# Optimization experiments

Hardware: AMD Instinct MI355X
Metric: run time of the kernel (lower is better)

Reference implementation:

```python
import jax, jax.numpy as jnp
import numpy as np

H, DM, N, K, R = 768, 1536, 16, 4, 48  # hidden, intermediate, state, conv kernel, dt rank
B, L = 2, 1024


def _silu(x):
    return x * jax.nn.sigmoid(x)


def _causal_conv(x, w, b):
    # x: [B, D, L]; w: [D, K] depthwise; causal left-pad K-1 (matches causal_conv1d_fn)
    out = jax.lax.conv_general_dilated(
        x, w[:, None, :], window_strides=(1,), padding=[(K - 1, 0)],
        feature_group_count=w.shape[0], dimension_numbers=('NCH', 'OIH', 'NCH'))
    return out + b[None, :, None]


def _selective_scan(u, delta, A, Bm, Cm, Dp, gate):
    # u/delta/gate: [B, D, L]; A: [D, N]; Bm/Cm: [B, L, N]; Dp: [D]
    dA = jnp.exp(delta[:, :, :, None] * A[None, :, None, :])              # [B,D,L,N]
    dBu = delta[:, :, :, None] * Bm[:, None, :, :] * u[:, :, :, None]      # [B,D,L,N]
    dA_t = jnp.moveaxis(dA, 2, 0)    # [L,B,D,N]
    dBu_t = jnp.moveaxis(dBu, 2, 0)  # [L,B,D,N]
    C_t = jnp.moveaxis(Cm, 1, 0)     # [L,B,N]

    def step(x, inp):
        a, bu, c = inp
        x = a * x + bu                               # [B,D,N]
        y = jnp.einsum('bdn,bn->bd', x, c)
        return x, y

    x0 = jnp.zeros(dA_t.shape[1:], dA_t.dtype)
    _, ys = jax.lax.scan(step, x0, (dA_t, dBu_t, C_t))
    y = jnp.moveaxis(ys, 0, 2) + u * Dp[None, :, None]   # [B,D,L]
    return y * _silu(gate)


def _branch(conv_out, gate, xw, dtw, dtb, Alog, Dp):
    # conv_out/gate: [B, D, L]
    ssm = jnp.einsum('bdl,pd->blp', conv_out, xw)        # [B,L,R+2N]
    ts, Bm, Cm = ssm[..., :R], ssm[..., R:R + N], ssm[..., R + N:]
    delta = jax.nn.softplus(jnp.einsum('dr,blr->bdl', dtw, ts) + dtb[None, :, None])
    A = -jnp.exp(Alog)
    return _selective_scan(conv_out, delta, A, Bm, Cm, Dp, gate)


def setup_inputs() -> dict:
    key = jax.random.key(0)
    ks = jax.random.split(key, 12)
    s = 0.02
    hidden_states = jax.random.normal(ks[0], (B, L, H), jnp.float32)
    in_proj_w = jax.random.normal(ks[1], (2 * DM, H), jnp.float32) * s
    conv_w = jax.random.normal(ks[2], (DM, K), jnp.float32) * 0.3
    conv_b = jax.random.normal(ks[3], (DM,), jnp.float32) * s
    x_proj_w = jax.random.normal(ks[4], (R + 2 * N, DM), jnp.float32) * s
    dt_proj_w = jax.random.normal(ks[5], (DM, R), jnp.float32) * s
    dt_proj_b = -4.0 + 0.1 * jax.random.normal(ks[6], (DM,), jnp.float32)
    x_proj_back_w = jax.random.normal(ks[7], (R + 2 * N, DM), jnp.float32) * s
    dt_proj_back_w = jax.random.normal(ks[8], (DM, R), jnp.float32) * s
    dt_proj_back_b = -4.0 + 0.1 * jax.random.normal(ks[9], (DM,), jnp.float32)
    A_log = jnp.log(jnp.broadcast_to(jnp.arange(1, N + 1, dtype=jnp.float32)[None, :], (DM, N)))
    A_log_back = A_log
    D = jnp.ones((DM,), jnp.float32)
    D_back = jnp.ones((DM,), jnp.float32)
    out_proj_w = jax.random.normal(ks[10], (H, DM), jnp.float32) * s
    return {
        'hidden_states': hidden_states, 'in_proj_w': in_proj_w,
        'conv_w': conv_w, 'conv_b': conv_b,
        'x_proj_w': x_proj_w, 'dt_proj_w': dt_proj_w, 'dt_proj_b': dt_proj_b,
        'x_proj_back_w': x_proj_back_w, 'dt_proj_back_w': dt_proj_back_w,
        'dt_proj_back_b': dt_proj_back_b, 'A_log': A_log, 'A_log_back': A_log_back,
        'D': D, 'D_back': D_back, 'out_proj_w': out_proj_w,
    }


def reference(hidden_states, in_proj_w, conv_w, conv_b, x_proj_w, dt_proj_w,
              dt_proj_b, x_proj_back_w, dt_proj_back_w, dt_proj_back_b,
              A_log, A_log_back, D, D_back, out_proj_w):
    proj = jnp.einsum('blh,ph->bpl', hidden_states, in_proj_w)  # [B,2D,L]
    x, gate = proj[:, :DM], proj[:, DM:]
    conv_out = _silu(_causal_conv(x, conv_w, conv_b))           # [B,D,L]
    # forward-direction scan
    y_f = _branch(conv_out, gate, x_proj_w, dt_proj_w, dt_proj_b, A_log, D)
    # backward-direction scan on time-flipped conv output and gate
    y_b = _branch(conv_out[:, :, ::-1], gate[:, :, ::-1], x_proj_back_w,
                  dt_proj_back_w, dt_proj_back_b, A_log_back, D_back)
    y = y_f + y_b[:, :, ::-1]
    return jnp.einsum('bdl,hd->blh', y, out_proj_w)
```

## Files before the change

### kernel.cpp

```cpp
#include <hip/hip_runtime.h>
#include <math.h>

constexpr int cH  = 768;
constexpr int cDM = 1536;
constexpr int cN  = 16;
constexpr int cR  = 48;
constexpr int cB  = 2;
constexpr int cL  = 1024;
constexpr int cPS = 160;
constexpr int cCK = 32;

typedef unsigned short u16;
typedef __attribute__((ext_vector_type(8))) short bf16x8;
typedef __attribute__((ext_vector_type(4))) float f32x4;

__device__ __forceinline__ u16 f2bf(float f) {
    unsigned u = __float_as_uint(f);
    u += 0x7FFF + ((u >> 16) & 1);
    return (u16)(u >> 16);
}
__device__ __forceinline__ float bf2f(u16 h) {
    return __uint_as_float((unsigned)h << 16);
}
__device__ __forceinline__ float fexp2(float x) {
    float r; asm("v_exp_f32 %0, %1" : "=v"(r) : "v"(x)); return r;
}
constexpr float cLOG2E = 1.44269504f;

__global__ __launch_bounds__(256)
void prep_kernel(const float* __restrict__ hid, const float* __restrict__ inw,
                 const float* __restrict__ xpw, const float* __restrict__ xpbw,
                 const float* __restrict__ outw, const float* __restrict__ dtw,
                 const float* __restrict__ dtbw,
                 u16* __restrict__ hid_b, u16* __restrict__ inw_b,
                 u16* __restrict__ xpw2_b, u16* __restrict__ outw_b,
                 u16* __restrict__ dtw2_b)
{
    const long i8 = ((long)blockIdx.x * 256 + threadIdx.x) * 8;
    const long e0 = 1572864;
    const long e1 = e0 + 2359296;
    const long e2 = e1 + 122880;
    const long e3 = e2 + 122880;
    const long e4 = e3 + 1179648;
    const long e5 = e4 + 98304;
    const long e6 = e5 + 98304;
    const float* in; u16* out; long off; int pad = 0;
    if      (i8 < e0) { in = hid;  out = hid_b;           off = i8; }
    else if (i8 < e1) { in = inw;  out = inw_b;           off = i8 - e0; }
    else if (i8 < e2) { in = xpw;  out = xpw2_b;          off = i8 - e1; }
    else if (i8 < e3) { in = xpbw; out = xpw2_b + 122880; off = i8 - e2; }
    else if (i8 < e4) { in = outw; out = outw_b;          off = i8 - e3; }
    else if (i8 < e5) { in = dtw;  out = dtw2_b;          off = i8 - e4; pad = 1; }
    else if (i8 < e6) { in = dtbw; out = dtw2_b + 98304;  off = i8 - e5; pad = 1; }
    else return;
    u16 o[8];
    if (!pad) {
        const float4 a = *(const float4*)&in[off];
        const float4 b = *(const float4*)&in[off + 4];
        o[0]=f2bf(a.x); o[1]=f2bf(a.y); o[2]=f2bf(a.z); o[3]=f2bf(a.w);
        o[4]=f2bf(b.x); o[5]=f2bf(b.y); o[6]=f2bf(b.z); o[7]=f2bf(b.w);
    } else {
        const long r = off >> 6; const int k0 = (int)(off & 63);
        #pragma unroll
        for (int k = 0; k < 8; ++k)
            o[k] = (k0 + k < cR) ? f2bf(in[r * cR + k0 + k]) : (u16)0;
    }
    *(uint4*)&out[off] = *(uint4*)o;
}

__global__ __launch_bounds__(256)
void tspad_kernel(const float* __restrict__ ssms, u16* __restrict__ out) {
    int i = blockIdx.x * 256 + threadIdx.x;
    int dirsel = i >> 17;
    int rem = i & 131071;
    int bl = rem >> 6, k = rem & 63;
    out[i] = (k < cR) ? f2bf(ssms[(long)bl * cPS + dirsel * 80 + k]) : (u16)0;
}

__global__ __launch_bounds__(256)
void comb_kernel(u16* __restrict__ yf, const u16* __restrict__ yb, long n8) {
    long i = (long)blockIdx.x * 256 + threadIdx.x;
    if (i >= n8) return;
    uint4 av = ((uint4*)yf)[i];
    uint4 bv = ((const uint4*)yb)[i];
    unsigned* ap = (unsigned*)&av;
    unsigned* bp = (unsigned*)&bv;
    #pragma unroll
    for (int j = 0; j < 4; ++j) {
        const float lo = bf2f((u16)(ap[j] & 0xffff)) + bf2f((u16)(bp[j] & 0xffff));
        const float hi = bf2f((u16)(ap[j] >> 16))    + bf2f((u16)(bp[j] >> 16));
        ap[j] = (unsigned)f2bf(lo) | ((unsigned)f2bf(hi) << 16);
    }
    ((uint4*)yf)[i] = av;
}

__device__ __forceinline__ void gld_lds16(const u16* g, u16* l) {
    __builtin_amdgcn_global_load_lds(
        (const __attribute__((address_space(1))) unsigned int*)g,
        (__attribute__((address_space(3))) unsigned int*)l, 16, 0, 0);
}

#define GST(SA, SB, k0) do {                                                   \
    _Pragma("unroll")                                                          \
    for (int h = 0; h < 3; ++h) {                                              \
        const int q  = wid * 3 + h;                                            \
        const int rw = lane >> 2;                                              \
        if (q < 4) {                                                           \
            const int r  = q * 16 + rw;                                        \
            const int sw = (r & 3) ^ ((r >> 2) & 3);                           \
            const int kg = (k0) + (((lane & 3) ^ sw) << 3);                    \
            gld_lds16(Ab + (long)(m0 + r) * lda + kg, &SA[q * 512]);           \
        } else {                                                               \
            const int r  = (q - 4) * 16 + rw;                                  \
            const int sw = (r & 3) ^ ((r >> 2) & 3);                           \
            const int kg = (k0) + (((lane & 3) ^ sw) << 3);                    \
            int nr = n0 + r; if (nr > N2 - 1) nr = N2 - 1;                     \
            gld_lds16(Bb + (long)nr * ldb + kg, &SB[(q - 4) * 512]);           \
        }                                                                      \
    }                                                                          \
} while (0)

#define CMP(SA, SB) do {                                                       \
    bf16x8 af[4], bfr[2];                                                      \
    _Pragma("unroll")                                                          \
    for (int i = 0; i < 4; ++i) {                                              \
        const int ra  = i * 16 + lr;                                           \
        const int swa = (ra & 3) ^ ((ra >> 2) & 3);                            \
        af[i] = *(const bf16x8*)&SA[ra * 32 + ((lc ^ swa) << 3)];              \
    }                                                                          \
    _Pragma("unroll")                                                          \
    for (int j = 0; j < 2; ++j) {                                              \
        const int rb  = wn + j * 16 + lr;                                      \
        const int swb = (rb & 3) ^ ((rb >> 2) & 3);                            \
        bfr[j] = *(const bf16x8*)&SB[rb * 32 + ((lc ^ swb) << 3)];             \
    }                                                                          \
    _Pragma("unroll")                                                          \
    for (int i = 0; i < 4; ++i)                                                \
        _Pragma("unroll")                                                      \
        for (int j = 0; j < 2; ++j)                                            \
            acc[i][j] = __builtin_amdgcn_mfma_f32_16x16x32_bf16(af[i], bfr[j], acc[i][j], 0, 0, 0); \
} while (0)

template<int EPI>
__global__ __launch_bounds__(256, 4)
void gemm_mfma(const u16* __restrict__ A, const u16* __restrict__ B,
               float* __restrict__ C0, float* __restrict__ C1,
               const float* __restrict__ bias,
               int N2, int Kd, int lda, int ldb, int ldc,
               long sA, long sC, int splitCol, int kspl)
{
    __shared__ __align__(16) u16 shA0[2048];
    __shared__ __align__(16) u16 shA1[2048];
    __shared__ __align__(16) u16 shB0[4096];
    __shared__ __align__(16) u16 shB1[4096];
    const int tid  = threadIdx.x;
    const int wid  = tid >> 6, lane = tid & 63;
    const int lr   = lane & 15, lc = lane >> 4;
    const int z    = blockIdx.z;
    const int bz   = z / kspl, ks = z % kspl;
    const int kpc  = Kd / kspl;
    const int kbeg = ks * kpc;
    const int nt   = kpc / 32;
    const int n0 = blockIdx.x * 128, m0 = blockIdx.y * 64;
    const int wn = wid * 32;

    const u16* Ab = A + (long)bz * sA;
    const u16* Bb = B;

    f32x4 acc[4][2] = {};

    GST(shA0, shB0, kbeg);
    __syncthreads();
    int t = 0;
    for (;;) {
        if (t + 1 < nt) GST(shA1, shB1, kbeg + (t + 1) * 32);
        CMP(shA0, shB0);
        __syncthreads();
        if (++t >= nt) break;
        if (t + 1 < nt) GST(shA0, shB0, kbeg + (t + 1) * 32);
        CMP(shA1, shB1);
        __syncthreads();
        if (++t >= nt) break;
    }

    #pragma unroll
    for (int i = 0; i < 4; ++i) {
        #pragma unroll
        for (int e = 0; e < 4; ++e) {
            const int m = m0 + i * 16 + lc * 4 + e;
            float* base0 = C0 + (long)bz * sC + (long)m * ldc;
            float* base1 = (C1 != nullptr) ? C1 + (long)bz * sC + (long)m * ldc : nullptr;
            #pragma unroll
            for (int j = 0; j < 2; ++j) {
                const int n = n0 + wn + j * 16 + lr;
                if (n < N2) {
                    float v = acc[i][j][e];
                    if (EPI == 1) {
                        const float t2 = v + bias[n];
                        v = fmaxf(t2, 0.f) + __logf(1.f + __expf(-fabsf(t2)));
                    }
                    float* cp = (base1 && n >= splitCol) ? base1 + (n - splitCol)
                                                         : base0 + n;
                    if (EPI == 2) atomicAdd(cp, v);
                    else          *cp = v;
                }
            }
        }
    }
}

__global__ __launch_bounds__(256)
void conv_silu2(const float* __restrict__ x, const float* __restrict__ cw,
                const float* __restrict__ cb,
                float* __restrict__ convTf, u16* __restrict__ convT_b)
{
    __shared__ float xt[35][64];
    const int l0 = blockIdx.x * 32, d0 = blockIdx.y * 64, b = blockIdx.z;
    const int tid = threadIdx.x;
    for (int i = tid; i < 35 * 64; i += 256) {
        const int r = i >> 6, c = i & 63;
        const int l = l0 - 3 + r;
        xt[r][c] = (l >= 0) ? x[((long)b * cL + l) * cDM + d0 + c] : 0.f;
    }
    __syncthreads();
    const int dc = tid & 63, lsub = tid >> 6;
    const int d = d0 + dc;
    const float w0 = cw[d*4], w1 = cw[d*4+1], w2 = cw[d*4+2], w3 = cw[d*4+3];
    const float bi = cb[d];
    #pragma unroll
    for (int k = 0; k < 8; ++k) {
        const int row = lsub * 8 + k;
        float v = bi;
        v = fmaf(w0, xt[row][dc],     v);
        v = fmaf(w1, xt[row + 1][dc], v);
        v = fmaf(w2, xt[row + 2][dc], v);
        v = fmaf(w3, xt[row + 3][dc], v);
        const float s = v / (1.f + __expf(-v));
        const long o = ((long)b * cL + l0 + row) * cDM + d;
        convTf[o] = s;
        convT_b[o] = f2bf(s);
    }
}

#define SA_LOAD(g, DU, UU) _Pragma("unroll")                                   \
    for (int k = 0; k < 4; ++k) {                                              \
        const int t_ = (g) * 4 + k;                                            \
        const int l_ = dir ? (base - t_) : (base + t_);                        \
        DU[k] = dT[(long)l_ * cDM + d]; UU[k] = uT[(long)l_ * cDM + d];        \
    }

#define SA_COMP(g, DU, UU) _Pragma("unroll")                                   \
    for (int k = 0; k < 4; ++k) {                                              \
        const int t_ = (g) * 4 + k;                                            \
        const float du_ = DU[k]; const float duu_ = du_ * UU[k];               \
        sdu += du_;                                                            \
        const float4 b0_ = *(const float4*)&bcA[t_][half * 8];                 \
        const float4 b1_ = *(const float4*)&bcA[t_][half * 8 + 4];             \
        const float bb_[8] = {b0_.x,b0_.y,b0_.z,b0_.w,b1_.x,b1_.y,b1_.z,b1_.w};\
        _Pragma("unroll")                                                      \
        for (int n = 0; n < 8; ++n)                                            \
            xs[n] = fmaf(fexp2(du_ * a2[n]), xs[n], duu_ * bb_[n]);            \
    }

__global__ __launch_bounds__(64, 4)
void scanA_kernel(const float* __restrict__ dT0, const float* __restrict__ dT1,
                  const float* __restrict__ uF, const float* __restrict__ ssms,
                  const float* __restrict__ AlogF, const float* __restrict__ AlogB,
                  float* __restrict__ Ap_out, float* __restrict__ Xf_out)
{
    __shared__ float bcA[32][16];
    const int lane = threadIdx.x;
    const int dd = lane & 31, half = lane >> 5;
    const int d = blockIdx.x * 32 + dd;
    const int b = blockIdx.y;
    const int z = blockIdx.z;
    const int dir = z >> 5, ck = z & 31;
    const float* Alog = dir ? AlogB : AlogF;
    const float* dT = (dir ? dT1 : dT0) + (long)b * cL * cDM;
    const float* uT = uF + (long)b * cL * cDM;
    const float* sp = ssms + (long)b * cL * cPS;
    const int sofs = dir ? 128 : 48;
    const int base = dir ? (cL - 1 - ck * 32) : (ck * 32);

    #pragma unroll
    for (int h = 0; h < 2; ++h) {
        const int idx = h * 64 + lane;
        const int r = idx >> 2, q = idx & 3;
        const int lr_ = dir ? (base - r) : (base + r);
        *(float4*)&bcA[r][q * 4] = *(const float4*)&sp[(long)lr_ * cPS + sofs + q * 4];
    }
    float a2[8];
    {
        const float4 a0 = *(const float4*)&Alog[d * 16 + half * 8];
        const float4 a1 = *(const float4*)&Alog[d * 16 + half * 8 + 4];
        a2[0]=-__expf(a0.x)*cLOG2E; a2[1]=-__expf(a0.y)*cLOG2E;
        a2[2]=-__expf(a0.z)*cLOG2E; a2[3]=-__expf(a0.w)*cLOG2E;
        a2[4]=-__expf(a1.x)*cLOG2E; a2[5]=-__expf(a1.y)*cLOG2E;
        a2[6]=-__expf(a1.z)*cLOG2E; a2[7]=-__expf(a1.w)*cLOG2E;
    }
    __syncthreads();

    float xs[8] = {};
    float sdu = 0.f;

    float dX[4], uX[4], dY[4], uY[4], dZ[4], uZ[4];
    SA_LOAD(0, dX, uX);
    SA_LOAD(1, dY, uY);
    SA_LOAD(2, dZ, uZ);
    SA_COMP(0, dX, uX); SA_LOAD(3, dX, uX);
    SA_COMP(1, dY, uY); SA_LOAD(4, dY, uY);
    SA_COMP(2, dZ, uZ); SA_LOAD(5, dZ, uZ);
    SA_COMP(3, dX, uX); SA_LOAD(6, dX, uX);
    SA_COMP(4, dY, uY); SA_LOAD(7, dY, uY);
    SA_COMP(5, dZ, uZ);
    SA_COMP(6, dX, uX);
    SA_COMP(7, dY, uY);

    const long ob = (((long)(b * 2 + dir) * cCK + ck) * cDM + d) * 16 + half * 8;
    *(float4*)&Ap_out[ob]     = make_float4(fexp2(sdu*a2[0]), fexp2(sdu*a2[1]),
                                            fexp2(sdu*a2[2]), fexp2(sdu*a2[3]));
    *(float4*)&Ap_out[ob + 4] = make_float4(fexp2(sdu*a2[4]), fexp2(sdu*a2[5]),
                                            fexp2(sdu*a2[6]), fexp2(sdu*a2[7]));
    *(float4*)&Xf_out[ob]     = make_float4(xs[0], xs[1], xs[2], xs[3]);
    *(float4*)&Xf_out[ob + 4] = make_float4(xs[4], xs[5], xs[6], xs[7]);
}

__global__ __launch_bounds__(256)
void scanB_kernel(float* __restrict__ Ap, const float* __restrict__ Xf)
{
    const int gid = blockIdx.x * 256 + threadIdx.x;
    const int n = gid & 15;
    const int rest = gid >> 4;
    const int d = rest % cDM;
    const int b2 = rest / cDM;
    float x0 = 0.f;
    #pragma unroll
    for (int c = 0; c < cCK; ++c) {
        const long idx = (((long)b2 * cCK + c) * cDM + d) * 16 + n;
        const float ap = Ap[idx], xf = Xf[idx];
        Ap[idx] = x0;
        x0 = fmaf(ap, x0, xf);
    }
}

#define SC_LOAD(g, DU, UU, GV) _Pragma("unroll")                               \
    for (int k = 0; k < 4; ++k) {                                              \
        const int t_ = (g) * 4 + k;                                            \
        const int l_ = dir ? (base - t_) : (base + t_);                        \
        const long off_ = (long)l_ * cDM + d;                                  \
        DU[k] = dT[off_]; UU[k] = uT[off_]; GV[k] = gT[off_];                  \
    }

#define SC_COMP(g, DU, UU, GV) _Pragma("unroll")                               \
    for (int k = 0; k < 4; ++k) {                                              \
        const int t_ = (g) * 4 + k;                                            \
        const float du_ = DU[k]; const float uu_ = UU[k];                      \
        const float duu_ = du_ * uu_;                                          \
        const float4 b0_ = *(const float4*)&bc[t_][half * 8];                  \
        const float4 b1_ = *(const float4*)&bc[t_][half * 8 + 4];              \
        const float4 c0_ = *(const float4*)&bc[t_][16 + half * 8];             \
        const float4 c1_ = *(const float4*)&bc[t_][16 + half * 8 + 4];         \
        const float bb_[8] = {b0_.x,b0_.y,b0_.z,b0_.w,b1_.x,b1_.y,b1_.z,b1_.w};\
        const float cc_[8] = {c0_.x,c0_.y,c0_.z,c0_.w,c1_.x,c1_.y,c1_.z,c1_.w};\
        float y_ = 0.f;                                                        \
        _Pragma("unroll")                                                      \
        for (int n = 0; n < 8; ++n) {                                          \
            xs[n] = fmaf(fexp2(du_ * a2[n]), xs[n], duu_ * bb_[n]);            \
            y_ = fmaf(xs[n], cc_[n], y_);                                      \
        }                                                                      \
        y_ += __shfl_xor(y_, 32);                                              \
        if (half == 0) {                                                       \
            const int l2_ = dir ? (base - t_) : (base + t_);                   \
            const float gv_ = GV[k];                                           \
            const float val_ = (y_ + uu_ * Dd) * (gv_ / (1.f + __expf(-gv_))); \
            yout[((long)b * cL + l2_) * cDM + d] = f2bf(val_);                 \
        }                                                                      \
    }

__global__ __launch_bounds__(64, 4)
void scanC_kernel(const float* __restrict__ dT0, const float* __restrict__ dT1,
                  const float* __restrict__ uF, const float* __restrict__ gF,
                  const float* __restrict__ ssms,
                  const float* __restrict__ AlogF, const float* __restrict__ AlogB,
                  const float* __restrict__ Df, const float* __restrict__ Db,
                  const float* __restrict__ X0,
                  u16* __restrict__ yf, u16* __restrict__ yb)
{
    __shared__ float bc[32][32];
    const int lane = threadIdx.x;
    const int dd = lane & 31, half = lane >> 5;
    const int d = blockIdx.x * 32 + dd;
    const int b = blockIdx.y;
    const int z = blockIdx.z;
    const int dir = z >> 5, ck = z & 31;
    const float* Alog = dir ? AlogB : AlogF;
    const float* dT = (dir ? dT1 : dT0) + (long)b * cL * cDM;
    const float* uT = uF + (long)b * cL * cDM;
    const float* gT = gF + (long)b * cL * cDM;
    const float* sp = ssms + (long)b * cL * cPS;
    const float Dd = dir ? Db[d] : Df[d];
    u16* yout = dir ? yb : yf;
    const int sofs = dir ? 128 : 48;
    const int base = dir ? (cL - 1 - ck * 32) : (ck * 32);

    #pragma unroll
    for (int h = 0; h < 4; ++h) {
        const int idx = h * 64 + lane;
        const int r = idx >> 3, q = idx & 7;
        const int lr_ = dir ? (base - r) : (base + r);
        *(float4*)&bc[r][q * 4] = *(const float4*)&sp[(long)lr_ * cPS + sofs + q * 4];
    }
    float a2[8];
    {
        const float4 a0 = *(const float4*)&Alog[d * 16 + half * 8];
        const float4 a1 = *(const float4*)&Alog[d * 16 + half * 8 + 4];
        a2[0]=-__expf(a0.x)*cLOG2E; a2[1]=-__expf(a0.y)*cLOG2E;
        a2[2]=-__expf(a0.z)*cLOG2E; a2[3]=-__expf(a0.w)*cLOG2E;
        a2[4]=-__expf(a1.x)*cLOG2E; a2[5]=-__expf(a1.y)*cLOG2E;
        a2[6]=-__expf(a1.z)*cLOG2E; a2[7]=-__expf(a1.w)*cLOG2E;
    }
    float xs[8];
    {
        const long ob = (((long)(b * 2 + dir) * cCK + ck) * cDM + d) * 16 + half * 8;
        const float4 x0v = *(const float4*)&X0[ob];
        const float4 x1v = *(const float4*)&X0[ob + 4];
        xs[0]=x0v.x; xs[1]=x0v.y; xs[2]=x0v.z; xs[3]=x0v.w;
        xs[4]=x1v.x; xs[5]=x1v.y; xs[6]=x1v.z; xs[7]=x1v.w;
    }
    __syncthreads();

    float dX[4], uX[4], gX[4], dY[4], uY[4], gY[4], dZ[4], uZ[4], gZ[4];
    SC_LOAD(0, dX, uX, gX);
    SC_LOAD(1, dY, uY, gY);
    SC_LOAD(2, dZ, uZ, gZ);
    SC_COMP(0, dX, uX, gX); SC_LOAD(3, dX, uX, gX);
    SC_COMP(1, dY, uY, gY); SC_LOAD(4, dY, uY, gY);
    SC_COMP(2, dZ, uZ, gZ); SC_LOAD(5, dZ, uZ, gZ);
    SC_COMP(3, dX, uX, gX); SC_LOAD(6, dX, uX, gX);
    SC_COMP(4, dY, uY, gY); SC_LOAD(7, dY, uY, gY);
    SC_COMP(5, dZ, uZ, gZ);
    SC_COMP(6, dX, uX, gX);
    SC_COMP(7, dY, uY, gY);
}

extern "C" void kernel_launch(void* const* d_in, const int* in_sizes, int n_in,
                              void* d_out, int out_size, void* d_ws, size_t ws_size,
                              hipStream_t stream)
{
    const float* hid   = (const float*)d_in[0];
    const float* inw   = (const float*)d_in[1];
    const float* convw = (const float*)d_in[2];
    const float* convb = (const float*)d_in[3];
    const float* xpw   = (const float*)d_in[4];
    const float* dtw   = (const float*)d_in[5];
    const float* dtb   = (const float*)d_in[6];
    const float* xpbw  = (const float*)d_in[7];
    const float* dtbw  = (const float*)d_in[8];
    const float* dtbb  = (const float*)d_in[9];
    const float* Alog  = (const float*)d_in[10];
    const float* Alogb = (const float*)d_in[11];
    const float* Dv    = (const float*)d_in[12];
    const float* Dbv   = (const float*)d_in[13];
    const float* outw  = (const float*)d_in[14];
    float* out = (float*)d_out;

    float* ws = (float*)d_ws;
    const long S = (long)cB * cDM * cL;
    float* xbuf   = ws;
    float* gate   = ws + S;
    float* convTf = ws + 2 * S;
    float* deltaT1= ws + 3 * S;
    float* ssms   = ws + 4 * S;
    u16* up0      = (u16*)(ssms + (long)cB * cL * cPS);
    u16* convT_b  = up0;
    u16* ts2_b    = up0 + S;
    u16* xpw2_b   = ts2_b + (long)2 * cB * cL * 64;
    u16* dtw2_b   = xpw2_b + (long)cPS * cDM;
    u16* outw_b   = dtw2_b + (long)2 * cDM * 64;
    u16* pool2    = outw_b + (long)cH * cDM;
    u16* inw_b    = pool2;
    u16* hid_b    = pool2 + (long)2 * cDM * cH;
    u16* yf_b     = convT_b;
    u16* yb_b     = pool2;
    const long nSum = (long)2 * cB * cCK * cDM * 16;
    float* sumAp  = (float*)(pool2 + 3932160);
    float* sumXf  = sumAp + nSum;

    const dim3 blk(256);

    prep_kernel<<<dim3(2713), blk, 0, stream>>>(
        hid, inw, xpw, xpbw, outw, dtw, dtbw,
        hid_b, inw_b, xpw2_b, outw_b, dtw2_b);

    hipMemsetAsync(ssms, 0, (long)cB * cL * cPS * sizeof(float), stream);
    hipMemsetAsync(out, 0, (long)out_size * sizeof(float), stream);

    gemm_mfma<0><<<dim3(24, 16, cB), blk, 0, stream>>>(
        hid_b, inw_b, xbuf, gate, nullptr,
        2 * cDM, cH, cH, cH, cDM, (long)cL * cH, (long)cL * cDM, cDM, 1);

    conv_silu2<<<dim3(32, 24, cB), blk, 0, stream>>>(
        xbuf, convw, convb, convTf, convT_b);

    gemm_mfma<2><<<dim3(2, 16, cB * 8), blk, 0, stream>>>(
        convT_b, xpw2_b, ssms, nullptr, nullptr,
        cPS, cDM, cDM, cDM, cPS, (long)cL * cDM, (long)cL * cPS, 1 << 30, 8);

    tspad_kernel<<<1024, blk, 0, stream>>>(ssms, ts2_b);

    gemm_mfma<1><<<dim3(12, 16, cB), blk, 0, stream>>>(
        ts2_b, dtw2_b, xbuf, nullptr, dtb,
        cDM, 64, 64, 64, cDM, (long)cL * 64, (long)cL * cDM, 1 << 30, 1);
    gemm_mfma<1><<<dim3(12, 16, cB), blk, 0, stream>>>(
        ts2_b + (long)2 * cL * 64, dtw2_b + (long)cDM * 64, deltaT1, nullptr, dtbb,
        cDM, 64, 64, 64, cDM, (long)cL * 64, (long)cL * cDM, 1 << 30, 1);

    scanA_kernel<<<dim3(48, cB, 2 * cCK), dim3(64), 0, stream>>>(
        xbuf, deltaT1, convTf, ssms, Alog, Alogb, sumAp, sumXf);
    scanB_kernel<<<dim3(384), blk, 0, stream>>>(sumAp, sumXf);
    scanC_kernel<<<dim3(48, cB, 2 * cCK), dim3(64), 0, stream>>>(
        xbuf, deltaT1, convTf, gate, ssms, Alog, Alogb, Dv, Dbv,
        sumAp , yf_b, yb_b);

    comb_kernel<<<(int)(S / 8 / 256), blk, 0, stream>>>(yf_b, yb_b, S / 8);

    gemm_mfma<2><<<dim3(6, 16, cB * 2), blk, 0, stream>>>(
        yf_b, outw_b, out, nullptr, nullptr,
        cH, cDM, cDM, cDM, cH, (long)cL * cDM, (long)cL * cH, 1 << 30, 2);
}
```

Baseline: 170.3 us.

## Store delta, conv output and silu(gate) as bf16 intermediates for the scan kernels

The in-projection GEMM epilogue now writes silu(gate) directly as bf16, and the dt-projection GEMM writes its softplus delta as bf16. The scan kernels read bf16 delta, conv output and precomputed silu(gate) instead of fp32 buffers, and the fp32 conv output copy is dropped. This halves the bytes the memory-bound scan passes have to read and removes a sigmoid from the scan's inner loop. The load prefetch depth in scanA and scanC is raised from three groups to four. The risk is accuracy loss from bf16 delta and u in the exponentials of the recurrence.

```diff
diff --git a/kernel.cpp b/kernel.cpp
--- a/kernel.cpp
+++ b/kernel.cpp
@@ -144,7 +144,7 @@
 template<int EPI>
 __global__ __launch_bounds__(256, 4)
 void gemm_mfma(const u16* __restrict__ A, const u16* __restrict__ B,
-               float* __restrict__ C0, float* __restrict__ C1,
+               void* __restrict__ C0v, void* __restrict__ C1v,
                const float* __restrict__ bias,
                int N2, int Kd, int lda, int ldb, int ldc,
                long sA, long sC, int splitCol, int kspl)
@@ -188,21 +188,25 @@
         #pragma unroll
         for (int e = 0; e < 4; ++e) {
             const int m = m0 + i * 16 + lc * 4 + e;
-            float* base0 = C0 + (long)bz * sC + (long)m * ldc;
-            float* base1 = (C1 != nullptr) ? C1 + (long)bz * sC + (long)m * ldc : nullptr;
+            const long rowoff = (long)bz * sC + (long)m * ldc;
             #pragma unroll
             for (int j = 0; j < 2; ++j) {
                 const int n = n0 + wn + j * 16 + lr;
                 if (n < N2) {
                     float v = acc[i][j][e];
-                    if (EPI == 1) {
+                    if (EPI == 2) {
+                        atomicAdd((float*)C0v + rowoff + n, v);
+                    } else if (EPI == 3) {
                         const float t2 = v + bias[n];
-                        v = fmaxf(t2, 0.f) + __logf(1.f + __expf(-fabsf(t2)));
+                        const float sp = fmaxf(t2, 0.f) + __logf(1.f + __expf(-fabsf(t2)));
+                        ((u16*)C0v)[rowoff + n] = f2bf(sp);
+                    } else {
+                        if (n < splitCol)
+                            ((float*)C0v)[rowoff + n] = v;
+                        else
+                            ((u16*)C1v)[rowoff + (n - splitCol)] =
+                                f2bf(v / (1.f + __expf(-v)));
                     }
-                    float* cp = (base1 && n >= splitCol) ? base1 + (n - splitCol)
-                                                         : base0 + n;
-                    if (EPI == 2) atomicAdd(cp, v);
-                    else          *cp = v;
                 }
             }
         }
@@ -211,8 +215,7 @@
 
 __global__ __launch_bounds__(256)
 void conv_silu2(const float* __restrict__ x, const float* __restrict__ cw,
-                const float* __restrict__ cb,
-                float* __restrict__ convTf, u16* __restrict__ convT_b)
+                const float* __restrict__ cb, u16* __restrict__ convT_b)
 {
     __shared__ float xt[35][64];
     const int l0 = blockIdx.x * 32, d0 = blockIdx.y * 64, b = blockIdx.z;
@@ -236,9 +239,7 @@
         v = fmaf(w2, xt[row + 2][dc], v);
         v = fmaf(w3, xt[row + 3][dc], v);
         const float s = v / (1.f + __expf(-v));
-        const long o = ((long)b * cL + l0 + row) * cDM + d;
-        convTf[o] = s;
-        convT_b[o] = f2bf(s);
+        convT_b[((long)b * cL + l0 + row) * cDM + d] = f2bf(s);
     }
 }
 
@@ -246,7 +247,8 @@
     for (int k = 0; k < 4; ++k) {                                              \
         const int t_ = (g) * 4 + k;                                            \
         const int l_ = dir ? (base - t_) : (base + t_);                        \
-        DU[k] = dT[(long)l_ * cDM + d]; UU[k] = uT[(long)l_ * cDM + d];        \
+        const long off_ = (long)l_ * cDM + d;                                  \
+        DU[k] = bf2f(dTb[off_]); UU[k] = bf2f(uTb[off_]);                      \
     }
 
 #define SA_COMP(g, DU, UU) _Pragma("unroll")                                   \
@@ -263,8 +265,8 @@
     }
 
 __global__ __launch_bounds__(64, 4)
-void scanA_kernel(const float* __restrict__ dT0, const float* __restrict__ dT1,
-                  const float* __restrict__ uF, const float* __restrict__ ssms,
+void scanA_kernel(const u16* __restrict__ dT0, const u16* __restrict__ dT1,
+                  const u16* __restrict__ uB, const float* __restrict__ ssms,
                   const float* __restrict__ AlogF, const float* __restrict__ AlogB,
                   float* __restrict__ Ap_out, float* __restrict__ Xf_out)
 {
@@ -276,8 +278,8 @@
     const int z = blockIdx.z;
     const int dir = z >> 5, ck = z & 31;
     const float* Alog = dir ? AlogB : AlogF;
-    const float* dT = (dir ? dT1 : dT0) + (long)b * cL * cDM;
-    const float* uT = uF + (long)b * cL * cDM;
+    const u16* dTb = (dir ? dT1 : dT0) + (long)b * cL * cDM;
+    const u16* uTb = uB + (long)b * cL * cDM;
     const float* sp = ssms + (long)b * cL * cPS;
     const int sofs = dir ? 128 : 48;
     const int base = dir ? (cL - 1 - ck * 32) : (ck * 32);
@@ -303,18 +305,19 @@
     float xs[8] = {};
     float sdu = 0.f;
 
-    float dX[4], uX[4], dY[4], uY[4], dZ[4], uZ[4];
+    float dX[4], uX[4], dY[4], uY[4], dZ[4], uZ[4], dW[4], uW[4];
     SA_LOAD(0, dX, uX);
     SA_LOAD(1, dY, uY);
     SA_LOAD(2, dZ, uZ);
-    SA_COMP(0, dX, uX); SA_LOAD(3, dX, uX);
-    SA_COMP(1, dY, uY); SA_LOAD(4, dY, uY);
-    SA_COMP(2, dZ, uZ); SA_LOAD(5, dZ, uZ);
-    SA_COMP(3, dX, uX); SA_LOAD(6, dX, uX);
-    SA_COMP(4, dY, uY); SA_LOAD(7, dY, uY);
-    SA_COMP(5, dZ, uZ);
-    SA_COMP(6, dX, uX);
-    SA_COMP(7, dY, uY);
+    SA_LOAD(3, dW, uW);
+    SA_COMP(0, dX, uX); SA_LOAD(4, dX, uX);
+    SA_COMP(1, dY, uY); SA_LOAD(5, dY, uY);
+    SA_COMP(2, dZ, uZ); SA_LOAD(6, dZ, uZ);
+    SA_COMP(3, dW, uW); SA_LOAD(7, dW, uW);
+    SA_COMP(4, dX, uX);
+    SA_COMP(5, dY, uY);
+    SA_COMP(6, dZ, uZ);
+    SA_COMP(7, dW, uW);
 
     const long ob = (((long)(b * 2 + dir) * cCK + ck) * cDM + d) * 16 + half * 8;
     *(float4*)&Ap_out[ob]     = make_float4(fexp2(sdu*a2[0]), fexp2(sdu*a2[1]),
@@ -343,15 +346,16 @@
     }
 }
 
-#define SC_LOAD(g, DU, UU, GV) _Pragma("unroll")                               \
+#define SC_LOAD(g, DU, UU, SG) _Pragma("unroll")                               \
     for (int k = 0; k < 4; ++k) {                                              \
         const int t_ = (g) * 4 + k;                                            \
         const int l_ = dir ? (base - t_) : (base + t_);                        \
         const long off_ = (long)l_ * cDM + d;                                  \
-        DU[k] = dT[off_]; UU[k] = uT[off_]; GV[k] = gT[off_];                  \
-    }
-
-#define SC_COMP(g, DU, UU, GV) _Pragma("unroll")                               \
+        DU[k] = bf2f(dTb[off_]); UU[k] = bf2f(uTb[off_]);                      \
+        if (half == 0) SG[k] = bf2f(sgb[off_]);                                \
+    }
+
+#define SC_COMP(g, DU, UU, SG) _Pragma("unroll")                               \
     for (int k = 0; k < 4; ++k) {                                              \
         const int t_ = (g) * 4 + k;                                            \
         const float du_ = DU[k]; const float uu_ = UU[k];                      \
@@ -371,15 +375,14 @@
         y_ += __shfl_xor(y_, 32);                                              \
         if (half == 0) {                                                       \
             const int l2_ = dir ? (base - t_) : (base + t_);                   \
-            const float gv_ = GV[k];                                           \
-            const float val_ = (y_ + uu_ * Dd) * (gv_ / (1.f + __expf(-gv_))); \
+            const float val_ = (y_ + uu_ * Dd) * SG[k];                        \
             yout[((long)b * cL + l2_) * cDM + d] = f2bf(val_);                 \
         }                                                                      \
     }
 
 __global__ __launch_bounds__(64, 4)
-void scanC_kernel(const float* __restrict__ dT0, const float* __restrict__ dT1,
-                  const float* __restrict__ uF, const float* __restrict__ gF,
+void scanC_kernel(const u16* __restrict__ dT0, const u16* __restrict__ dT1,
+                  const u16* __restrict__ uB, const u16* __restrict__ sgB,
                   const float* __restrict__ ssms,
                   const float* __restrict__ AlogF, const float* __restrict__ AlogB,
                   const float* __restrict__ Df, const float* __restrict__ Db,
@@ -394,9 +397,9 @@
     const int z = blockIdx.z;
     const int dir = z >> 5, ck = z & 31;
     const float* Alog = dir ? AlogB : AlogF;
-    const float* dT = (dir ? dT1 : dT0) + (long)b * cL * cDM;
-    const float* uT = uF + (long)b * cL * cDM;
-    const float* gT = gF + (long)b * cL * cDM;
+    const u16* dTb = (dir ? dT1 : dT0) + (long)b * cL * cDM;
+    const u16* uTb = uB + (long)b * cL * cDM;
+    const u16* sgb = sgB + (long)b * cL * cDM;
     const float* sp = ssms + (long)b * cL * cPS;
     const float Dd = dir ? Db[d] : Df[d];
     u16* yout = dir ? yb : yf;
@@ -429,18 +432,20 @@
     }
     __syncthreads();
 
-    float dX[4], uX[4], gX[4], dY[4], uY[4], gY[4], dZ[4], uZ[4], gZ[4];
+    float dX[4], uX[4], gX[4], dY[4], uY[4], gY[4];
+    float dZ[4], uZ[4], gZ[4], dW[4], uW[4], gW[4];
     SC_LOAD(0, dX, uX, gX);
     SC_LOAD(1, dY, uY, gY);
     SC_LOAD(2, dZ, uZ, gZ);
-    SC_COMP(0, dX, uX, gX); SC_LOAD(3, dX, uX, gX);
-    SC_COMP(1, dY, uY, gY); SC_LOAD(4, dY, uY, gY);
-    SC_COMP(2, dZ, uZ, gZ); SC_LOAD(5, dZ, uZ, gZ);
-    SC_COMP(3, dX, uX, gX); SC_LOAD(6, dX, uX, gX);
-    SC_COMP(4, dY, uY, gY); SC_LOAD(7, dY, uY, gY);
-    SC_COMP(5, dZ, uZ, gZ);
-    SC_COMP(6, dX, uX, gX);
-    SC_COMP(7, dY, uY, gY);
+    SC_LOAD(3, dW, uW, gW);
+    SC_COMP(0, dX, uX, gX); SC_LOAD(4, dX, uX, gX);
+    SC_COMP(1, dY, uY, gY); SC_LOAD(5, dY, uY, gY);
+    SC_COMP(2, dZ, uZ, gZ); SC_LOAD(6, dZ, uZ, gZ);
+    SC_COMP(3, dW, uW, gW); SC_LOAD(7, dW, uW, gW);
+    SC_COMP(4, dX, uX, gX);
+    SC_COMP(5, dY, uY, gY);
+    SC_COMP(6, dZ, uZ, gZ);
+    SC_COMP(7, dW, uW, gW);
 }
 
 extern "C" void kernel_launch(void* const* d_in, const int* in_sizes, int n_in,
@@ -466,25 +471,24 @@
 
     float* ws = (float*)d_ws;
     const long S = (long)cB * cDM * cL;
+    const long nSum = (long)2 * cB * cCK * cDM * 16;
     float* xbuf   = ws;
-    float* gate   = ws + S;
-    float* convTf = ws + 2 * S;
-    float* deltaT1= ws + 3 * S;
-    float* ssms   = ws + 4 * S;
-    u16* up0      = (u16*)(ssms + (long)cB * cL * cPS);
-    u16* convT_b  = up0;
-    u16* ts2_b    = up0 + S;
+    float* ssms   = ws + S;
+    float* sumAp  = ssms + (long)cB * cL * cPS;
+    float* sumXf  = sumAp + nSum;
+    u16* ub       = (u16*)(sumXf + nSum);
+    u16* convT_b  = ub;
+    u16* sg_b     = convT_b + S;
+    u16* d0_b     = sg_b + S;
+    u16* d1_b     = d0_b + S;
+    u16* yf_b     = d1_b + S;
+    u16* yb_b     = yf_b + S;
+    u16* ts2_b    = yb_b + S;
     u16* xpw2_b   = ts2_b + (long)2 * cB * cL * 64;
     u16* dtw2_b   = xpw2_b + (long)cPS * cDM;
     u16* outw_b   = dtw2_b + (long)2 * cDM * 64;
-    u16* pool2    = outw_b + (long)cH * cDM;
-    u16* inw_b    = pool2;
-    u16* hid_b    = pool2 + (long)2 * cDM * cH;
-    u16* yf_b     = convT_b;
-    u16* yb_b     = pool2;
-    const long nSum = (long)2 * cB * cCK * cDM * 16;
-    float* sumAp  = (float*)(pool2 + 3932160);
-    float* sumXf  = sumAp + nSum;
+    u16* inw_b    = outw_b + (long)cH * cDM;
+    u16* hid_b    = inw_b + (long)2 * cDM * cH;
 
     const dim3 blk(256);
 
@@ -495,12 +499,12 @@
     hipMemsetAsync(ssms, 0, (long)cB * cL * cPS * sizeof(float), stream);
     hipMemsetAsync(out, 0, (long)out_size * sizeof(float), stream);
 
-    gemm_mfma<0><<<dim3(24, 16, cB), blk, 0, stream>>>(
-        hid_b, inw_b, xbuf, gate, nullptr,
+    gemm_mfma<4><<<dim3(24, 16, cB), blk, 0, stream>>>(
+        hid_b, inw_b, xbuf, sg_b, nullptr,
         2 * cDM, cH, cH, cH, cDM, (long)cL * cH, (long)cL * cDM, cDM, 1);
 
     conv_silu2<<<dim3(32, 24, cB), blk, 0, stream>>>(
-        xbuf, convw, convb, convTf, convT_b);
+        xbuf, convw, convb, convT_b);
 
     gemm_mfma<2><<<dim3(2, 16, cB * 8), blk, 0, stream>>>(
         convT_b, xpw2_b, ssms, nullptr, nullptr,
@@ -508,18 +512,18 @@
 
     tspad_kernel<<<1024, blk, 0, stream>>>(ssms, ts2_b);
 
-    gemm_mfma<1><<<dim3(12, 16, cB), blk, 0, stream>>>(
-        ts2_b, dtw2_b, xbuf, nullptr, dtb,
+    gemm_mfma<3><<<dim3(12, 16, cB), blk, 0, stream>>>(
+        ts2_b, dtw2_b, d0_b, nullptr, dtb,
         cDM, 64, 64, 64, cDM, (long)cL * 64, (long)cL * cDM, 1 << 30, 1);
-    gemm_mfma<1><<<dim3(12, 16, cB), blk, 0, stream>>>(
-        ts2_b + (long)2 * cL * 64, dtw2_b + (long)cDM * 64, deltaT1, nullptr, dtbb,
+    gemm_mfma<3><<<dim3(12, 16, cB), blk, 0, stream>>>(
+        ts2_b + (long)2 * cL * 64, dtw2_b + (long)cDM * 64, d1_b, nullptr, dtbb,
         cDM, 64, 64, 64, cDM, (long)cL * 64, (long)cL * cDM, 1 << 30, 1);
 
     scanA_kernel<<<dim3(48, cB, 2 * cCK), dim3(64), 0, stream>>>(
-        xbuf, deltaT1, convTf, ssms, Alog, Alogb, sumAp, sumXf);
+        d0_b, d1_b, convT_b, ssms, Alog, Alogb, sumAp, sumXf);
     scanB_kernel<<<dim3(384), blk, 0, stream>>>(sumAp, sumXf);
     scanC_kernel<<<dim3(48, cB, 2 * cCK), dim3(64), 0, stream>>>(
-        xbuf, deltaT1, convTf, gate, ssms, Alog, Alogb, Dv, Dbv,
+        d0_b, d1_b, convT_b, sg_b, ssms, Alog, Alogb, Dv, Dbv,
         sumAp , yf_b, yb_b);
 
     comb_kernel<<<(int)(S / 8 / 256), blk, 0, stream>>>(yf_b, yb_b, S / 8);
```

After: 176.5 us. 1.04x slower.

## Fuse gate SiLU into in_proj epilogue and pack four scan chunks per block

Applied to the files above, without the earlier changes.

The in_proj GEMM gets a new epilogue that writes x directly and silu(gate) to a separate buffer, so the scanC kernel no longer recomputes the gate sigmoid and only half the lanes load it. scanA and scanC now run four independent 64-thread chunk scans per 256-thread block, each with its own shared slice, and the block barrier is dropped. The workspace layout is reorganised so yf/yb/sum buffers no longer alias the pooled bf16 weight copies. Dropping __syncthreads relies on each wave only reading shared data it wrote itself, and the larger blocks change occupancy and scheduling.

```diff
diff --git a/kernel.cpp b/kernel.cpp
--- a/kernel.cpp
+++ b/kernel.cpp
@@ -195,14 +195,15 @@
                 const int n = n0 + wn + j * 16 + lr;
                 if (n < N2) {
                     float v = acc[i][j][e];
-                    if (EPI == 1) {
+                    if (EPI == 4) {
+                        if (n < splitCol) base0[n] = v;
+                        else base1[n - splitCol] = v / (1.f + __expf(-v));
+                    } else if (EPI == 1) {
                         const float t2 = v + bias[n];
-                        v = fmaxf(t2, 0.f) + __logf(1.f + __expf(-fabsf(t2)));
+                        base0[n] = fmaxf(t2, 0.f) + __logf(1.f + __expf(-fabsf(t2)));
+                    } else {
+                        atomicAdd(base0 + n, v);
                     }
-                    float* cp = (base1 && n >= splitCol) ? base1 + (n - splitCol)
-                                                         : base0 + n;
-                    if (EPI == 2) atomicAdd(cp, v);
-                    else          *cp = v;
                 }
             }
         }
@@ -246,7 +247,8 @@
     for (int k = 0; k < 4; ++k) {                                              \
         const int t_ = (g) * 4 + k;                                            \
         const int l_ = dir ? (base - t_) : (base + t_);                        \
-        DU[k] = dT[(long)l_ * cDM + d]; UU[k] = uT[(long)l_ * cDM + d];        \
+        const long off_ = (long)l_ * cDM + d;                                  \
+        DU[k] = dT[off_]; UU[k] = uT[off_];                                    \
     }
 
 #define SA_COMP(g, DU, UU) _Pragma("unroll")                                   \
@@ -254,40 +256,42 @@
         const int t_ = (g) * 4 + k;                                            \
         const float du_ = DU[k]; const float duu_ = du_ * UU[k];               \
         sdu += du_;                                                            \
-        const float4 b0_ = *(const float4*)&bcA[t_][half * 8];                 \
-        const float4 b1_ = *(const float4*)&bcA[t_][half * 8 + 4];             \
+        const float4 b0_ = *(const float4*)&bca[t_][half * 8];                 \
+        const float4 b1_ = *(const float4*)&bca[t_][half * 8 + 4];             \
         const float bb_[8] = {b0_.x,b0_.y,b0_.z,b0_.w,b1_.x,b1_.y,b1_.z,b1_.w};\
         _Pragma("unroll")                                                      \
         for (int n = 0; n < 8; ++n)                                            \
             xs[n] = fmaf(fexp2(du_ * a2[n]), xs[n], duu_ * bb_[n]);            \
     }
 
-__global__ __launch_bounds__(64, 4)
+__global__ __launch_bounds__(256, 4)
 void scanA_kernel(const float* __restrict__ dT0, const float* __restrict__ dT1,
                   const float* __restrict__ uF, const float* __restrict__ ssms,
                   const float* __restrict__ AlogF, const float* __restrict__ AlogB,
                   float* __restrict__ Ap_out, float* __restrict__ Xf_out)
 {
-    __shared__ float bcA[32][16];
-    const int lane = threadIdx.x;
+    __shared__ float bcA[4][32][16];
+    const int tid = threadIdx.x;
+    const int w = tid >> 6, lane = tid & 63;
     const int dd = lane & 31, half = lane >> 5;
     const int d = blockIdx.x * 32 + dd;
     const int b = blockIdx.y;
-    const int z = blockIdx.z;
-    const int dir = z >> 5, ck = z & 31;
+    const int zs = blockIdx.z * 4 + w;
+    const int dir = zs >> 5, ck = zs & 31;
     const float* Alog = dir ? AlogB : AlogF;
     const float* dT = (dir ? dT1 : dT0) + (long)b * cL * cDM;
     const float* uT = uF + (long)b * cL * cDM;
     const float* sp = ssms + (long)b * cL * cPS;
     const int sofs = dir ? 128 : 48;
     const int base = dir ? (cL - 1 - ck * 32) : (ck * 32);
+    float (*bca)[16] = bcA[w];
 
     #pragma unroll
     for (int h = 0; h < 2; ++h) {
         const int idx = h * 64 + lane;
         const int r = idx >> 2, q = idx & 3;
         const int lr_ = dir ? (base - r) : (base + r);
-        *(float4*)&bcA[r][q * 4] = *(const float4*)&sp[(long)lr_ * cPS + sofs + q * 4];
+        *(float4*)&bca[r][q * 4] = *(const float4*)&sp[(long)lr_ * cPS + sofs + q * 4];
     }
     float a2[8];
     {
@@ -298,7 +302,6 @@
         a2[4]=-__expf(a1.x)*cLOG2E; a2[5]=-__expf(a1.y)*cLOG2E;
         a2[6]=-__expf(a1.z)*cLOG2E; a2[7]=-__expf(a1.w)*cLOG2E;
     }
-    __syncthreads();
 
     float xs[8] = {};
     float sdu = 0.f;
@@ -343,23 +346,24 @@
     }
 }
 
-#define SC_LOAD(g, DU, UU, GV) _Pragma("unroll")                               \
+#define SC_LOAD(g, DU, UU, SG) _Pragma("unroll")                               \
     for (int k = 0; k < 4; ++k) {                                              \
         const int t_ = (g) * 4 + k;                                            \
         const int l_ = dir ? (base - t_) : (base + t_);                        \
         const long off_ = (long)l_ * cDM + d;                                  \
-        DU[k] = dT[off_]; UU[k] = uT[off_]; GV[k] = gT[off_];                  \
-    }
-
-#define SC_COMP(g, DU, UU, GV) _Pragma("unroll")                               \
+        DU[k] = dT[off_]; UU[k] = uT[off_];                                    \
+        if (half == 0) SG[k] = sgp[off_];                                      \
+    }
+
+#define SC_COMP(g, DU, UU, SG) _Pragma("unroll")                               \
     for (int k = 0; k < 4; ++k) {                                              \
         const int t_ = (g) * 4 + k;                                            \
         const float du_ = DU[k]; const float uu_ = UU[k];                      \
         const float duu_ = du_ * uu_;                                          \
-        const float4 b0_ = *(const float4*)&bc[t_][half * 8];                  \
-        const float4 b1_ = *(const float4*)&bc[t_][half * 8 + 4];              \
-        const float4 c0_ = *(const float4*)&bc[t_][16 + half * 8];             \
-        const float4 c1_ = *(const float4*)&bc[t_][16 + half * 8 + 4];         \
+        const float4 b0_ = *(const float4*)&bcc[t_][half * 8];                 \
+        const float4 b1_ = *(const float4*)&bcc[t_][half * 8 + 4];             \
+        const float4 c0_ = *(const float4*)&bcc[t_][16 + half * 8];            \
+        const float4 c1_ = *(const float4*)&bcc[t_][16 + half * 8 + 4];        \
         const float bb_[8] = {b0_.x,b0_.y,b0_.z,b0_.w,b1_.x,b1_.y,b1_.z,b1_.w};\
         const float cc_[8] = {c0_.x,c0_.y,c0_.z,c0_.w,c1_.x,c1_.y,c1_.z,c1_.w};\
         float y_ = 0.f;                                                        \
@@ -371,44 +375,45 @@
         y_ += __shfl_xor(y_, 32);                                              \
         if (half == 0) {                                                       \
             const int l2_ = dir ? (base - t_) : (base + t_);                   \
-            const float gv_ = GV[k];                                           \
-            const float val_ = (y_ + uu_ * Dd) * (gv_ / (1.f + __expf(-gv_))); \
+            const float val_ = (y_ + uu_ * Dd) * SG[k];                        \
             yout[((long)b * cL + l2_) * cDM + d] = f2bf(val_);                 \
         }                                                                      \
     }
 
-__global__ __launch_bounds__(64, 4)
+__global__ __launch_bounds__(256, 4)
 void scanC_kernel(const float* __restrict__ dT0, const float* __restrict__ dT1,
-                  const float* __restrict__ uF, const float* __restrict__ gF,
+                  const float* __restrict__ uF, const float* __restrict__ sgF,
                   const float* __restrict__ ssms,
                   const float* __restrict__ AlogF, const float* __restrict__ AlogB,
                   const float* __restrict__ Df, const float* __restrict__ Db,
                   const float* __restrict__ X0,
                   u16* __restrict__ yf, u16* __restrict__ yb)
 {
-    __shared__ float bc[32][32];
-    const int lane = threadIdx.x;
+    __shared__ float bcS[4][32][32];
+    const int tid = threadIdx.x;
+    const int w = tid >> 6, lane = tid & 63;
     const int dd = lane & 31, half = lane >> 5;
     const int d = blockIdx.x * 32 + dd;
     const int b = blockIdx.y;
-    const int z = blockIdx.z;
-    const int dir = z >> 5, ck = z & 31;
+    const int zs = blockIdx.z * 4 + w;
+    const int dir = zs >> 5, ck = zs & 31;
     const float* Alog = dir ? AlogB : AlogF;
     const float* dT = (dir ? dT1 : dT0) + (long)b * cL * cDM;
     const float* uT = uF + (long)b * cL * cDM;
-    const float* gT = gF + (long)b * cL * cDM;
+    const float* sgp = sgF + (long)b * cL * cDM;
     const float* sp = ssms + (long)b * cL * cPS;
     const float Dd = dir ? Db[d] : Df[d];
     u16* yout = dir ? yb : yf;
     const int sofs = dir ? 128 : 48;
     const int base = dir ? (cL - 1 - ck * 32) : (ck * 32);
+    float (*bcc)[32] = bcS[w];
 
     #pragma unroll
     for (int h = 0; h < 4; ++h) {
         const int idx = h * 64 + lane;
         const int r = idx >> 3, q = idx & 7;
         const int lr_ = dir ? (base - r) : (base + r);
-        *(float4*)&bc[r][q * 4] = *(const float4*)&sp[(long)lr_ * cPS + sofs + q * 4];
+        *(float4*)&bcc[r][q * 4] = *(const float4*)&sp[(long)lr_ * cPS + sofs + q * 4];
     }
     float a2[8];
     {
@@ -427,7 +432,6 @@
         xs[0]=x0v.x; xs[1]=x0v.y; xs[2]=x0v.z; xs[3]=x0v.w;
         xs[4]=x1v.x; xs[5]=x1v.y; xs[6]=x1v.z; xs[7]=x1v.w;
     }
-    __syncthreads();
 
     float dX[4], uX[4], gX[4], dY[4], uY[4], gY[4], dZ[4], uZ[4], gZ[4];
     SC_LOAD(0, dX, uX, gX);
@@ -466,25 +470,24 @@
 
     float* ws = (float*)d_ws;
     const long S = (long)cB * cDM * cL;
+    const long nSum = (long)2 * cB * cCK * cDM * 16;
     float* xbuf   = ws;
-    float* gate   = ws + S;
+    float* sg     = ws + S;
     float* convTf = ws + 2 * S;
     float* deltaT1= ws + 3 * S;
     float* ssms   = ws + 4 * S;
-    u16* up0      = (u16*)(ssms + (long)cB * cL * cPS);
-    u16* convT_b  = up0;
-    u16* ts2_b    = up0 + S;
+    float* sumAp  = ssms + (long)cB * cL * cPS;
+    float* sumXf  = sumAp + nSum;
+    u16* ub       = (u16*)(sumXf + nSum);
+    u16* convT_b  = ub;
+    u16* yf_b     = convT_b + S;
+    u16* yb_b     = yf_b + S;
+    u16* ts2_b    = yb_b + S;
     u16* xpw2_b   = ts2_b + (long)2 * cB * cL * 64;
     u16* dtw2_b   = xpw2_b + (long)cPS * cDM;
     u16* outw_b   = dtw2_b + (long)2 * cDM * 64;
-    u16* pool2    = outw_b + (long)cH * cDM;
-    u16* inw_b    = pool2;
-    u16* hid_b    = pool2 + (long)2 * cDM * cH;
-    u16* yf_b     = convT_b;
-    u16* yb_b     = pool2;
-    const long nSum = (long)2 * cB * cCK * cDM * 16;
-    float* sumAp  = (float*)(pool2 + 3932160);
-    float* sumXf  = sumAp + nSum;
+    u16* inw_b    = outw_b + (long)cH * cDM;
+    u16* hid_b    = inw_b + (long)2 * cDM * cH;
 
     const dim3 blk(256);
 
@@ -495,8 +498,8 @@
     hipMemsetAsync(ssms, 0, (long)cB * cL * cPS * sizeof(float), stream);
     hipMemsetAsync(out, 0, (long)out_size * sizeof(float), stream);
 
-    gemm_mfma<0><<<dim3(24, 16, cB), blk, 0, stream>>>(
-        hid_b, inw_b, xbuf, gate, nullptr,
+    gemm_mfma<4><<<dim3(24, 16, cB), blk, 0, stream>>>(
+        hid_b, inw_b, xbuf, sg, nullptr,
         2 * cDM, cH, cH, cH, cDM, (long)cL * cH, (long)cL * cDM, cDM, 1);
 
     conv_silu2<<<dim3(32, 24, cB), blk, 0, stream>>>(
@@ -515,11 +518,11 @@
         ts2_b + (long)2 * cL * 64, dtw2_b + (long)cDM * 64, deltaT1, nullptr, dtbb,
         cDM, 64, 64, 64, cDM, (long)cL * 64, (long)cL * cDM, 1 << 30, 1);
 
-    scanA_kernel<<<dim3(48, cB, 2 * cCK), dim3(64), 0, stream>>>(
+    scanA_kernel<<<dim3(48, cB, 16), blk, 0, stream>>>(
         xbuf, deltaT1, convTf, ssms, Alog, Alogb, sumAp, sumXf);
     scanB_kernel<<<dim3(384), blk, 0, stream>>>(sumAp, sumXf);
-    scanC_kernel<<<dim3(48, cB, 2 * cCK), dim3(64), 0, stream>>>(
-        xbuf, deltaT1, convTf, gate, ssms, Alog, Alogb, Dv, Dbv,
+    scanC_kernel<<<dim3(48, cB, 16), blk, 0, stream>>>(
+        xbuf, deltaT1, convTf, sg, ssms, Alog, Alogb, Dv, Dbv,
         sumAp , yf_b, yb_b);
 
     comb_kernel<<<(int)(S / 8 / 256), blk, 0, stream>>>(yf_b, yb_b, S / 8);
```

Result: no change. 169.1 us (-0.7%).
